# Kernel tuning notes

Hardware: AMD Instinct MI355X
Metric: run time of the kernel (lower is better)

The kernel has to match this reference:

```python
import jax, jax.numpy as jnp
import numpy as np

N_EMBD = 1568  # 2 * 784, hard-coded in the source module
HEAD_SIZE = 128
BATCH = 16384


def setup_inputs() -> dict:
    key = jax.random.key(0)
    kx, kq, kk, kv = jax.random.split(key, 4)
    x = jax.random.normal(kx, (BATCH, N_EMBD), dtype=jnp.float32)
    wq = jax.random.normal(kq, (N_EMBD, HEAD_SIZE), dtype=jnp.float32) * (N_EMBD ** -0.5)
    wk = jax.random.normal(kk, (N_EMBD, HEAD_SIZE), dtype=jnp.float32) * (N_EMBD ** -0.5)
    wv = jax.random.normal(kv, (N_EMBD, HEAD_SIZE), dtype=jnp.float32) * (N_EMBD ** -0.5)
    return {"x": x, "wq": wq, "wk": wk, "wv": wv}


def reference(x, wq, wk, wv):
    # x: [B, N]; projections (bias-free Linear): [B, H]
    B, N = x.shape
    q = x @ wq
    k = x @ wk
    v = x @ wv
    # Outer-product score matrix per batch element: [B, H, H]
    attn = jnp.einsum('bi,bj->bij', q, k) * (N ** -0.5)  # scale uses FEATURE dim N, as in source
    attn = jax.nn.softmax(attn, axis=-1)
    # dropout is identity in eval mode
    out = jnp.einsum('bij,bj->bi', attn, v)  # [B, H]
    return out
```

## Files before the change

kernel.cpp:

```cpp
#include <hip/hip_runtime.h>
#include <stdint.h>

typedef unsigned short u16;
typedef __bf16 bf16x8 __attribute__((ext_vector_type(8)));
typedef float f32x4 __attribute__((ext_vector_type(4)));
typedef float f32x2 __attribute__((ext_vector_type(2)));

#define M_ROWS 16384
#define K_DIM  1568
#define H_DIM  128
#define NQ     384
#define MT     32
#define BK     32
#define NSTEP  49
#define CH_F   384
#define ASTR   392
#define TSTR   40
#define ABUF   (MT * ASTR)
#define PSTR   132
#define KSTRIDE (NQ * BK)
#define SCALE  0.02525381361380526f
#define LOG2E  1.4426950408889634f

__device__ __forceinline__ u16 f32_to_bf16_rne(float f) {
    uint32_t u = __float_as_uint(f);
    uint32_t r = (u + 0x7FFFu + ((u >> 16) & 1u)) >> 16;
    return (u16)r;
}

__device__ __forceinline__ uint32_t cvt_pk(float lo, float hi) {
    uint32_t d;
    asm("v_cvt_pk_bf16_f32 %0, %1, %2" : "=v"(d) : "v"(lo), "v"(hi));
    return d;
}

__device__ __forceinline__ f32x2 pk_mul(f32x2 a, f32x2 b) {
    f32x2 d; asm("v_pk_mul_f32 %0, %1, %2" : "=v"(d) : "v"(a), "v"(b)); return d;
}
__device__ __forceinline__ f32x2 pk_add(f32x2 a, f32x2 b) {
    f32x2 d; asm("v_pk_add_f32 %0, %1, %2" : "=v"(d) : "v"(a), "v"(b)); return d;
}
__device__ __forceinline__ f32x2 pk_fma(f32x2 a, f32x2 b, f32x2 c) {
    f32x2 d; asm("v_pk_fma_f32 %0, %1, %2, %3" : "=v"(d) : "v"(a), "v"(b), "v"(c)); return d;
}

__device__ __forceinline__ void cvt_wr8(u16* dst, f32x4 v) {
    uint2 t; t.x = cvt_pk(v.x, v.y); t.y = cvt_pk(v.z, v.w);
    *(uint2*)dst = t;
}

#define MFMA(a, b, c) __builtin_amdgcn_mfma_f32_16x16x32_bf16(a, b, c, 0, 0, 0)

__global__ __launch_bounds__(256) void wtrans_kernel(
    const float* __restrict__ wq, const float* __restrict__ wk,
    const float* __restrict__ wv, u16* __restrict__ wt2)
{
    __shared__ u16 tile[32][33];
    const float* w = (blockIdx.z == 0) ? wq : (blockIdx.z == 1) ? wk : wv;
    const int k0 = blockIdx.x * 32;
    const int nloc0 = blockIdx.y * 32;
    const int ng0 = blockIdx.z * 128 + nloc0;

    const int tn = threadIdx.x & 31;
    const int tk = threadIdx.x >> 5;
    #pragma unroll
    for (int p = 0; p < 4; p++) {
        int kk = tk + p * 8;
        tile[kk][tn] = f32_to_bf16_rne(w[(size_t)(k0 + kk) * H_DIM + nloc0 + tn]);
    }
    __syncthreads();

    const int klo = threadIdx.x & 31;
    const int tn2 = threadIdx.x >> 5;
    u16* dst = wt2 + (size_t)(k0 >> 5) * KSTRIDE;
    #pragma unroll
    for (int p = 0; p < 4; p++) {
        int nn = tn2 + p * 8;
        dst[(size_t)(ng0 + nn) * 32 + klo] = tile[klo][nn];
    }
}

__global__ __launch_bounds__(512, 4) void fused_kernel(
    const float* __restrict__ x,
    const u16* __restrict__ wt2,
    float* __restrict__ out)
{
    __shared__ char smem[2 * ABUF * 2 + MT * TSTR * 2];
    u16* A0 = (u16*)smem;
    u16* A1 = A0 + ABUF;
    u16* TB = A1 + ABUF;
    float (*Pq)[PSTR] = (float (*)[PSTR])smem;
    float (*Pk)[PSTR] = (float (*)[PSTR])(smem + MT * PSTR * 4);
    float (*Pv)[PSTR] = (float (*)[PSTR])(smem + 2 * MT * PSTR * 4);

    const int tid  = threadIdx.x;
    const int lane = tid & 63;
    const int wave = tid >> 6;
    const int lrow = lane & 15;
    const int quad = lane >> 4;
    const int m0   = blockIdx.x * MT;

    const u16* bp0 = wt2 + (size_t)(wave * 48 +  0 + lrow) * 32 + quad * 8;
    const u16* bp1 = wt2 + (size_t)(wave * 48 + 16 + lrow) * 32 + quad * 8;
    const u16* bp2 = wt2 + (size_t)(wave * 48 + 32 + lrow) * 32 + quad * 8;

    const int srow = tid >> 4;
    const int st16 = tid & 15;
    const float* xrow = x + (size_t)(m0 + srow) * K_DIM;
    u16* wb0 = A0 + srow * ASTR + st16 * 4;
    u16* wb1 = A1 + srow * ASTR + st16 * 4;

    const u16* aA0 = A0 + lrow * ASTR + quad * 8;
    const u16* aA1 = A0 + (16 + lrow) * ASTR + quad * 8;
    const u16* aB0 = A1 + lrow * ASTR + quad * 8;
    const u16* aB1 = A1 + (16 + lrow) * ASTR + quad * 8;

#define NTLD4(off) __builtin_nontemporal_load((const f32x4*)(xrow + (off)))
#define LOADC(S, OFF) do { \
    S##0 = NTLD4((OFF) + st16 * 4 +   0); \
    S##1 = NTLD4((OFF) + st16 * 4 +  64); \
    S##2 = NTLD4((OFF) + st16 * 4 + 128); \
    S##3 = NTLD4((OFF) + st16 * 4 + 192); \
    S##4 = NTLD4((OFF) + st16 * 4 + 256); \
    S##5 = NTLD4((OFF) + st16 * 4 + 320); \
} while (0)
#define WRITEC(WB, S) do { \
    cvt_wr8((WB) +   0, S##0); cvt_wr8((WB) +  64, S##1); \
    cvt_wr8((WB) + 128, S##2); cvt_wr8((WB) + 192, S##3); \
    cvt_wr8((WB) + 256, S##4); cvt_wr8((WB) + 320, S##5); \
} while (0)

    f32x4 acc00 = {}, acc01 = {}, acc02 = {};
    f32x4 acc10 = {}, acc11 = {}, acc12 = {};
    f32x4 s00, s01, s02, s03, s04, s05;
    f32x4 s10, s11, s12, s13, s14, s15;

    LOADC(s0, 0);
    f32x2 tl = __builtin_nontemporal_load((const f32x2*)(xrow + 1536 + st16 * 2));
    LOADC(s1, CH_F);
    WRITEC(wb0, s0);
    *(uint32_t*)(TB + srow * TSTR + st16 * 2) = cvt_pk(tl.x, tl.y);

    bf16x8 Ba0 = *(const bf16x8*)(bp0);
    bf16x8 Ba1 = *(const bf16x8*)(bp1);
    bf16x8 Ba2 = *(const bf16x8*)(bp2);
    bf16x8 Bb0 = *(const bf16x8*)(bp0 + KSTRIDE);
    bf16x8 Bb1 = *(const bf16x8*)(bp1 + KSTRIDE);
    bf16x8 Bb2 = *(const bf16x8*)(bp2 + KSTRIDE);
    __syncthreads();

#define KSTEP(P0, P1, IT, G) do { \
    int gp = (G) + 2; if (gp > NSTEP - 1) gp = NSTEP - 1; \
    const size_t o = (size_t)gp * KSTRIDE; \
    bf16x8 Bc0 = *(const bf16x8*)(bp0 + o); \
    bf16x8 Bc1 = *(const bf16x8*)(bp1 + o); \
    bf16x8 Bc2 = *(const bf16x8*)(bp2 + o); \
    bf16x8 a0 = *(const bf16x8*)((P0) + (IT) * BK); \
    bf16x8 a1 = *(const bf16x8*)((P1) + (IT) * BK); \
    acc00 = MFMA(a0, Ba0, acc00); acc10 = MFMA(a1, Ba0, acc10); \
    acc01 = MFMA(a0, Ba1, acc01); acc11 = MFMA(a1, Ba1, acc11); \
    acc02 = MFMA(a0, Ba2, acc02); acc12 = MFMA(a1, Ba2, acc12); \
    Ba0 = Bb0; Ba1 = Bb1; Ba2 = Bb2; Bb0 = Bc0; Bb1 = Bc1; Bb2 = Bc2; \
} while (0)

    WRITEC(wb1, s1);
    LOADC(s0, 2 * CH_F);
    #pragma unroll
    for (int it = 0; it < 12; ++it) KSTEP(aA0, aA1, it, it);
    __syncthreads();

    WRITEC(wb0, s0);
    LOADC(s1, 3 * CH_F);
    #pragma unroll
    for (int it = 0; it < 12; ++it) KSTEP(aB0, aB1, it, 12 + it);
    __syncthreads();

    WRITEC(wb1, s1);
    #pragma unroll
    for (int it = 0; it < 12; ++it) KSTEP(aA0, aA1, it, 24 + it);
    __syncthreads();

    #pragma unroll
    for (int it = 0; it < 12; ++it) KSTEP(aB0, aB1, it, 36 + it);

    {
        bf16x8 a0 = *(const bf16x8*)(TB + lrow * TSTR + quad * 8);
        bf16x8 a1 = *(const bf16x8*)(TB + (16 + lrow) * TSTR + quad * 8);
        acc00 = MFMA(a0, Ba0, acc00); acc10 = MFMA(a1, Ba0, acc10);
        acc01 = MFMA(a0, Ba1, acc01); acc11 = MFMA(a1, Ba1, acc11);
        acc02 = MFMA(a0, Ba2, acc02); acc12 = MFMA(a1, Ba2, acc12);
    }
    __syncthreads();

#define SCAT(ACC, MTi, NTi) do { \
    const int base = wave * 48 + (NTi) * 16; \
    const int sel  = base >> 7; \
    const int col  = (base & 127) + lrow; \
    const int mrow = (MTi) * 16 + quad * 4; \
    if (sel == 0)      { _Pragma("unroll") for (int rr = 0; rr < 4; rr++) Pq[mrow + rr][col] = ACC[rr] * (SCALE * LOG2E); } \
    else if (sel == 1) { _Pragma("unroll") for (int rr = 0; rr < 4; rr++) Pk[mrow + rr][col] = ACC[rr]; } \
    else               { _Pragma("unroll") for (int rr = 0; rr < 4; rr++) Pv[mrow + rr][col] = ACC[rr]; } \
} while (0)

    SCAT(acc00, 0, 0); SCAT(acc01, 0, 1); SCAT(acc02, 0, 2);
    SCAT(acc10, 1, 0); SCAT(acc11, 1, 1); SCAT(acc12, 1, 2);
    __syncthreads();

    const int r   = tid >> 4;
    const int sub = tid & 15;

    f32x4 qa = *(const f32x4*)&Pq[r][sub * 8];
    f32x4 qb = *(const f32x4*)&Pq[r][sub * 8 + 4];
    f32x2 q01; q01.x = qa.x; q01.y = qa.y;
    f32x2 q23; q23.x = qa.z; q23.y = qa.w;
    f32x2 q45; q45.x = qb.x; q45.y = qb.y;
    f32x2 q67; q67.x = qb.z; q67.y = qb.w;

    f32x2 d01 = {}, d23 = {}, d45 = {}, d67 = {};
    f32x2 n01 = {}, n23 = {}, n45 = {}, n67 = {};

    #pragma unroll 2
    for (int j4 = 0; j4 < 32; ++j4) {
        f32x4 k4 = *(const f32x4*)&Pk[r][j4 * 4];
        f32x4 v4 = *(const f32x4*)&Pv[r][j4 * 4];
        #pragma unroll
        for (int jj = 0; jj < 4; ++jj) {
            float kj = k4[jj];
            float vj = v4[jj];
            f32x2 kk; kk.x = kj; kk.y = kj;
            f32x2 vv; vv.x = vj; vv.y = vj;
            f32x2 sc01 = pk_mul(q01, kk);
            f32x2 sc23 = pk_mul(q23, kk);
            f32x2 sc45 = pk_mul(q45, kk);
            f32x2 sc67 = pk_mul(q67, kk);
            f32x2 e01; e01.x = __builtin_amdgcn_exp2f(sc01.x); e01.y = __builtin_amdgcn_exp2f(sc01.y);
            f32x2 e23; e23.x = __builtin_amdgcn_exp2f(sc23.x); e23.y = __builtin_amdgcn_exp2f(sc23.y);
            f32x2 e45; e45.x = __builtin_amdgcn_exp2f(sc45.x); e45.y = __builtin_amdgcn_exp2f(sc45.y);
            f32x2 e67; e67.x = __builtin_amdgcn_exp2f(sc67.x); e67.y = __builtin_amdgcn_exp2f(sc67.y);
            d01 = pk_add(d01, e01); n01 = pk_fma(e01, vv, n01);
            d23 = pk_add(d23, e23); n23 = pk_fma(e23, vv, n23);
            d45 = pk_add(d45, e45); n45 = pk_fma(e45, vv, n45);
            d67 = pk_add(d67, e67); n67 = pk_fma(e67, vv, n67);
        }
    }

    float* op = out + (size_t)(m0 + r) * H_DIM + sub * 8;
    f32x4 o0, o1;
    o0.x = n01.x / d01.x; o0.y = n01.y / d01.y;
    o0.z = n23.x / d23.x; o0.w = n23.y / d23.y;
    o1.x = n45.x / d45.x; o1.y = n45.y / d45.y;
    o1.z = n67.x / d67.x; o1.w = n67.y / d67.y;
    __builtin_nontemporal_store(o0, (f32x4*)(op));
    __builtin_nontemporal_store(o1, (f32x4*)(op + 4));
}

extern "C" void kernel_launch(void* const* d_in, const int* in_sizes, int n_in,
                              void* d_out, int out_size, void* d_ws, size_t ws_size,
                              hipStream_t stream)
{
    const float* x  = (const float*)d_in[0];
    const float* wq = (const float*)d_in[1];
    const float* wk = (const float*)d_in[2];
    const float* wv = (const float*)d_in[3];
    float* out = (float*)d_out;

    u16* wt2 = (u16*)d_ws;

    wtrans_kernel<<<dim3(K_DIM / 32, H_DIM / 32, 3), 256, 0, stream>>>(wq, wk, wv, wt2);
    fused_kernel<<<M_ROWS / MT, 512, 0, stream>>>(x, wt2, out);
}
```

Before: 204.1 us.

## Double the row tile to 64 and pipeline eight narrower K chunks

Raises the per-block row tile from 32 to 64 so each weight fragment loaded from global memory feeds twice as many MFMAs. This halves weight traffic per row and halves the block count. The K loop is restructured into eight 192-wide chunks with a double-buffered register/LDS pipeline, sized so the staging fits in the reused epilogue buffer. The softmax epilogue now has each thread handle 16 output columns. The cost is more accumulators and registers per thread, occupancy hints lowered from 4 to 2 blocks, and more barriers.

```diff
diff --git a/kernel.cpp b/kernel.cpp
--- a/kernel.cpp
+++ b/kernel.cpp
@@ -10,11 +10,12 @@
 #define K_DIM  1568
 #define H_DIM  128
 #define NQ     384
-#define MT     32
+#define MT     64
 #define BK     32
 #define NSTEP  49
-#define CH_F   384
-#define ASTR   392
+#define NCH    8
+#define CH_F   192
+#define ASTR   200
 #define TSTR   40
 #define ABUF   (MT * ASTR)
 #define PSTR   132
@@ -80,12 +81,12 @@
     }
 }
 
-__global__ __launch_bounds__(512, 4) void fused_kernel(
+__global__ __launch_bounds__(512, 2) void fused_kernel(
     const float* __restrict__ x,
     const u16* __restrict__ wt2,
     float* __restrict__ out)
 {
-    __shared__ char smem[2 * ABUF * 2 + MT * TSTR * 2];
+    __shared__ char smem[3 * MT * PSTR * 4];
     u16* A0 = (u16*)smem;
     u16* A1 = A0 + ABUF;
     u16* TB = A1 + ABUF;
@@ -104,42 +105,46 @@
     const u16* bp1 = wt2 + (size_t)(wave * 48 + 16 + lrow) * 32 + quad * 8;
     const u16* bp2 = wt2 + (size_t)(wave * 48 + 32 + lrow) * 32 + quad * 8;
 
-    const int srow = tid >> 4;
-    const int st16 = tid & 15;
+    const int srow = tid >> 3;
+    const int st8  = tid & 7;
     const float* xrow = x + (size_t)(m0 + srow) * K_DIM;
-    u16* wb0 = A0 + srow * ASTR + st16 * 4;
-    u16* wb1 = A1 + srow * ASTR + st16 * 4;
-
-    const u16* aA0 = A0 + lrow * ASTR + quad * 8;
-    const u16* aA1 = A0 + (16 + lrow) * ASTR + quad * 8;
-    const u16* aB0 = A1 + lrow * ASTR + quad * 8;
-    const u16* aB1 = A1 + (16 + lrow) * ASTR + quad * 8;
+    u16* wbs[2];
+    wbs[0] = A0 + srow * ASTR + st8 * 4;
+    wbs[1] = A1 + srow * ASTR + st8 * 4;
+
+    const u16* aF[2][4];
+    #pragma unroll
+    for (int m = 0; m < 4; m++) {
+        aF[0][m] = A0 + (m * 16 + lrow) * ASTR + quad * 8;
+        aF[1][m] = A1 + (m * 16 + lrow) * ASTR + quad * 8;
+    }
 
 #define NTLD4(off) __builtin_nontemporal_load((const f32x4*)(xrow + (off)))
 #define LOADC(S, OFF) do { \
-    S##0 = NTLD4((OFF) + st16 * 4 +   0); \
-    S##1 = NTLD4((OFF) + st16 * 4 +  64); \
-    S##2 = NTLD4((OFF) + st16 * 4 + 128); \
-    S##3 = NTLD4((OFF) + st16 * 4 + 192); \
-    S##4 = NTLD4((OFF) + st16 * 4 + 256); \
-    S##5 = NTLD4((OFF) + st16 * 4 + 320); \
+    S[0] = NTLD4((OFF) + st8 * 4 +   0); \
+    S[1] = NTLD4((OFF) + st8 * 4 +  32); \
+    S[2] = NTLD4((OFF) + st8 * 4 +  64); \
+    S[3] = NTLD4((OFF) + st8 * 4 +  96); \
+    S[4] = NTLD4((OFF) + st8 * 4 + 128); \
+    S[5] = NTLD4((OFF) + st8 * 4 + 160); \
 } while (0)
 #define WRITEC(WB, S) do { \
-    cvt_wr8((WB) +   0, S##0); cvt_wr8((WB) +  64, S##1); \
-    cvt_wr8((WB) + 128, S##2); cvt_wr8((WB) + 192, S##3); \
-    cvt_wr8((WB) + 256, S##4); cvt_wr8((WB) + 320, S##5); \
+    cvt_wr8((WB) +   0, S[0]); cvt_wr8((WB) +  32, S[1]); \
+    cvt_wr8((WB) +  64, S[2]); cvt_wr8((WB) +  96, S[3]); \
+    cvt_wr8((WB) + 128, S[4]); cvt_wr8((WB) + 160, S[5]); \
 } while (0)
 
     f32x4 acc00 = {}, acc01 = {}, acc02 = {};
     f32x4 acc10 = {}, acc11 = {}, acc12 = {};
-    f32x4 s00, s01, s02, s03, s04, s05;
-    f32x4 s10, s11, s12, s13, s14, s15;
-
-    LOADC(s0, 0);
-    f32x2 tl = __builtin_nontemporal_load((const f32x2*)(xrow + 1536 + st16 * 2));
-    LOADC(s1, CH_F);
-    WRITEC(wb0, s0);
-    *(uint32_t*)(TB + srow * TSTR + st16 * 2) = cvt_pk(tl.x, tl.y);
+    f32x4 acc20 = {}, acc21 = {}, acc22 = {};
+    f32x4 acc30 = {}, acc31 = {}, acc32 = {};
+    f32x4 sreg[2][6];
+
+    LOADC(sreg[0], 0);
+    f32x4 tl = NTLD4(1536 + st8 * 4);
+    LOADC(sreg[1], CH_F);
+    WRITEC(wbs[0], sreg[0]);
+    cvt_wr8(TB + srow * TSTR + st8 * 4, tl);
 
     bf16x8 Ba0 = *(const bf16x8*)(bp0);
     bf16x8 Ba1 = *(const bf16x8*)(bp1);
@@ -149,46 +154,45 @@
     bf16x8 Bb2 = *(const bf16x8*)(bp2 + KSTRIDE);
     __syncthreads();
 
-#define KSTEP(P0, P1, IT, G) do { \
+#define KSTEP(AP, IT, G) do { \
     int gp = (G) + 2; if (gp > NSTEP - 1) gp = NSTEP - 1; \
     const size_t o = (size_t)gp * KSTRIDE; \
     bf16x8 Bc0 = *(const bf16x8*)(bp0 + o); \
     bf16x8 Bc1 = *(const bf16x8*)(bp1 + o); \
     bf16x8 Bc2 = *(const bf16x8*)(bp2 + o); \
-    bf16x8 a0 = *(const bf16x8*)((P0) + (IT) * BK); \
-    bf16x8 a1 = *(const bf16x8*)((P1) + (IT) * BK); \
+    bf16x8 a0 = *(const bf16x8*)((AP)[0] + (IT) * BK); \
+    bf16x8 a1 = *(const bf16x8*)((AP)[1] + (IT) * BK); \
+    bf16x8 a2 = *(const bf16x8*)((AP)[2] + (IT) * BK); \
+    bf16x8 a3 = *(const bf16x8*)((AP)[3] + (IT) * BK); \
     acc00 = MFMA(a0, Ba0, acc00); acc10 = MFMA(a1, Ba0, acc10); \
+    acc20 = MFMA(a2, Ba0, acc20); acc30 = MFMA(a3, Ba0, acc30); \
     acc01 = MFMA(a0, Ba1, acc01); acc11 = MFMA(a1, Ba1, acc11); \
+    acc21 = MFMA(a2, Ba1, acc21); acc31 = MFMA(a3, Ba1, acc31); \
     acc02 = MFMA(a0, Ba2, acc02); acc12 = MFMA(a1, Ba2, acc12); \
+    acc22 = MFMA(a2, Ba2, acc22); acc32 = MFMA(a3, Ba2, acc32); \
     Ba0 = Bb0; Ba1 = Bb1; Ba2 = Bb2; Bb0 = Bc0; Bb1 = Bc1; Bb2 = Bc2; \
 } while (0)
 
-    WRITEC(wb1, s1);
-    LOADC(s0, 2 * CH_F);
-    #pragma unroll
-    for (int it = 0; it < 12; ++it) KSTEP(aA0, aA1, it, it);
-    __syncthreads();
-
-    WRITEC(wb0, s0);
-    LOADC(s1, 3 * CH_F);
-    #pragma unroll
-    for (int it = 0; it < 12; ++it) KSTEP(aB0, aB1, it, 12 + it);
-    __syncthreads();
-
-    WRITEC(wb1, s1);
-    #pragma unroll
-    for (int it = 0; it < 12; ++it) KSTEP(aA0, aA1, it, 24 + it);
-    __syncthreads();
-
-    #pragma unroll
-    for (int it = 0; it < 12; ++it) KSTEP(aB0, aB1, it, 36 + it);
+    #pragma unroll
+    for (int c = 0; c < NCH; ++c) {
+        if (c < NCH - 1) WRITEC(wbs[(c + 1) & 1], sreg[(c + 1) & 1]);
+        if (c < NCH - 2) LOADC(sreg[c & 1], (c + 2) * CH_F);
+        #pragma unroll
+        for (int it = 0; it < 6; ++it) KSTEP(aF[c & 1], it, c * 6 + it);
+        __syncthreads();
+    }
 
     {
-        bf16x8 a0 = *(const bf16x8*)(TB + lrow * TSTR + quad * 8);
-        bf16x8 a1 = *(const bf16x8*)(TB + (16 + lrow) * TSTR + quad * 8);
+        bf16x8 a0 = *(const bf16x8*)(TB + (lrow +  0) * TSTR + quad * 8);
+        bf16x8 a1 = *(const bf16x8*)(TB + (lrow + 16) * TSTR + quad * 8);
+        bf16x8 a2 = *(const bf16x8*)(TB + (lrow + 32) * TSTR + quad * 8);
+        bf16x8 a3 = *(const bf16x8*)(TB + (lrow + 48) * TSTR + quad * 8);
         acc00 = MFMA(a0, Ba0, acc00); acc10 = MFMA(a1, Ba0, acc10);
+        acc20 = MFMA(a2, Ba0, acc20); acc30 = MFMA(a3, Ba0, acc30);
         acc01 = MFMA(a0, Ba1, acc01); acc11 = MFMA(a1, Ba1, acc11);
+        acc21 = MFMA(a2, Ba1, acc21); acc31 = MFMA(a3, Ba1, acc31);
         acc02 = MFMA(a0, Ba2, acc02); acc12 = MFMA(a1, Ba2, acc12);
+        acc22 = MFMA(a2, Ba2, acc22); acc32 = MFMA(a3, Ba2, acc32);
     }
     __syncthreads();
 
@@ -204,20 +208,28 @@
 
     SCAT(acc00, 0, 0); SCAT(acc01, 0, 1); SCAT(acc02, 0, 2);
     SCAT(acc10, 1, 0); SCAT(acc11, 1, 1); SCAT(acc12, 1, 2);
-    __syncthreads();
-
-    const int r   = tid >> 4;
-    const int sub = tid & 15;
-
-    f32x4 qa = *(const f32x4*)&Pq[r][sub * 8];
-    f32x4 qb = *(const f32x4*)&Pq[r][sub * 8 + 4];
-    f32x2 q01; q01.x = qa.x; q01.y = qa.y;
-    f32x2 q23; q23.x = qa.z; q23.y = qa.w;
-    f32x2 q45; q45.x = qb.x; q45.y = qb.y;
-    f32x2 q67; q67.x = qb.z; q67.y = qb.w;
-
-    f32x2 d01 = {}, d23 = {}, d45 = {}, d67 = {};
-    f32x2 n01 = {}, n23 = {}, n45 = {}, n67 = {};
+    SCAT(acc20, 2, 0); SCAT(acc21, 2, 1); SCAT(acc22, 2, 2);
+    SCAT(acc30, 3, 0); SCAT(acc31, 3, 1); SCAT(acc32, 3, 2);
+    __syncthreads();
+
+    const int r   = tid >> 3;
+    const int sub = tid & 7;
+
+    f32x4 qa = *(const f32x4*)&Pq[r][sub * 16 +  0];
+    f32x4 qb = *(const f32x4*)&Pq[r][sub * 16 +  4];
+    f32x4 qc = *(const f32x4*)&Pq[r][sub * 16 +  8];
+    f32x4 qd = *(const f32x4*)&Pq[r][sub * 16 + 12];
+    f32x2 qp0; qp0.x = qa.x; qp0.y = qa.y;
+    f32x2 qp1; qp1.x = qa.z; qp1.y = qa.w;
+    f32x2 qp2; qp2.x = qb.x; qp2.y = qb.y;
+    f32x2 qp3; qp3.x = qb.z; qp3.y = qb.w;
+    f32x2 qp4; qp4.x = qc.x; qp4.y = qc.y;
+    f32x2 qp5; qp5.x = qc.z; qp5.y = qc.w;
+    f32x2 qp6; qp6.x = qd.x; qp6.y = qd.y;
+    f32x2 qp7; qp7.x = qd.z; qp7.y = qd.w;
+
+    f32x2 d0 = {}, d1 = {}, d2 = {}, d3 = {}, d4 = {}, d5 = {}, d6 = {}, d7 = {};
+    f32x2 n0 = {}, n1 = {}, n2 = {}, n3 = {}, n4 = {}, n5 = {}, n6 = {}, n7 = {};
 
     #pragma unroll 2
     for (int j4 = 0; j4 < 32; ++j4) {
@@ -229,29 +241,43 @@
             float vj = v4[jj];
             f32x2 kk; kk.x = kj; kk.y = kj;
             f32x2 vv; vv.x = vj; vv.y = vj;
-            f32x2 sc01 = pk_mul(q01, kk);
-            f32x2 sc23 = pk_mul(q23, kk);
-            f32x2 sc45 = pk_mul(q45, kk);
-            f32x2 sc67 = pk_mul(q67, kk);
-            f32x2 e01; e01.x = __builtin_amdgcn_exp2f(sc01.x); e01.y = __builtin_amdgcn_exp2f(sc01.y);
-            f32x2 e23; e23.x = __builtin_amdgcn_exp2f(sc23.x); e23.y = __builtin_amdgcn_exp2f(sc23.y);
-            f32x2 e45; e45.x = __builtin_amdgcn_exp2f(sc45.x); e45.y = __builtin_amdgcn_exp2f(sc45.y);
-            f32x2 e67; e67.x = __builtin_amdgcn_exp2f(sc67.x); e67.y = __builtin_amdgcn_exp2f(sc67.y);
-            d01 = pk_add(d01, e01); n01 = pk_fma(e01, vv, n01);
-            d23 = pk_add(d23, e23); n23 = pk_fma(e23, vv, n23);
-            d45 = pk_add(d45, e45); n45 = pk_fma(e45, vv, n45);
-            d67 = pk_add(d67, e67); n67 = pk_fma(e67, vv, n67);
+            f32x2 s0 = pk_mul(qp0, kk);
+            f32x2 s1 = pk_mul(qp1, kk);
+            f32x2 s2 = pk_mul(qp2, kk);
+            f32x2 s3 = pk_mul(qp3, kk);
+            f32x2 s4 = pk_mul(qp4, kk);
+            f32x2 s5 = pk_mul(qp5, kk);
+            f32x2 s6 = pk_mul(qp6, kk);
+            f32x2 s7 = pk_mul(qp7, kk);
+            f32x2 e0; e0.x = __builtin_amdgcn_exp2f(s0.x); e0.y = __builtin_amdgcn_exp2f(s0.y);
+            f32x2 e1; e1.x = __builtin_amdgcn_exp2f(s1.x); e1.y = __builtin_amdgcn_exp2f(s1.y);
+            f32x2 e2; e2.x = __builtin_amdgcn_exp2f(s2.x); e2.y = __builtin_amdgcn_exp2f(s2.y);
+            f32x2 e3; e3.x = __builtin_amdgcn_exp2f(s3.x); e3.y = __builtin_amdgcn_exp2f(s3.y);
+            f32x2 e4; e4.x = __builtin_amdgcn_exp2f(s4.x); e4.y = __builtin_amdgcn_exp2f(s4.y);
+            f32x2 e5; e5.x = __builtin_amdgcn_exp2f(s5.x); e5.y = __builtin_amdgcn_exp2f(s5.y);
+            f32x2 e6; e6.x = __builtin_amdgcn_exp2f(s6.x); e6.y = __builtin_amdgcn_exp2f(s6.y);
+            f32x2 e7; e7.x = __builtin_amdgcn_exp2f(s7.x); e7.y = __builtin_amdgcn_exp2f(s7.y);
+            d0 = pk_add(d0, e0); n0 = pk_fma(e0, vv, n0);
+            d1 = pk_add(d1, e1); n1 = pk_fma(e1, vv, n1);
+            d2 = pk_add(d2, e2); n2 = pk_fma(e2, vv, n2);
+            d3 = pk_add(d3, e3); n3 = pk_fma(e3, vv, n3);
+            d4 = pk_add(d4, e4); n4 = pk_fma(e4, vv, n4);
+            d5 = pk_add(d5, e5); n5 = pk_fma(e5, vv, n5);
+            d6 = pk_add(d6, e6); n6 = pk_fma(e6, vv, n6);
+            d7 = pk_add(d7, e7); n7 = pk_fma(e7, vv, n7);
         }
     }
 
-    float* op = out + (size_t)(m0 + r) * H_DIM + sub * 8;
-    f32x4 o0, o1;
-    o0.x = n01.x / d01.x; o0.y = n01.y / d01.y;
-    o0.z = n23.x / d23.x; o0.w = n23.y / d23.y;
-    o1.x = n45.x / d45.x; o1.y = n45.y / d45.y;
-    o1.z = n67.x / d67.x; o1.w = n67.y / d67.y;
-    __builtin_nontemporal_store(o0, (f32x4*)(op));
-    __builtin_nontemporal_store(o1, (f32x4*)(op + 4));
+    float* op = out + (size_t)(m0 + r) * H_DIM + sub * 16;
+    f32x4 o0, o1, o2, o3;
+    o0.x = n0.x / d0.x; o0.y = n0.y / d0.y; o0.z = n1.x / d1.x; o0.w = n1.y / d1.y;
+    o1.x = n2.x / d2.x; o1.y = n2.y / d2.y; o1.z = n3.x / d3.x; o1.w = n3.y / d3.y;
+    o2.x = n4.x / d4.x; o2.y = n4.y / d4.y; o2.z = n5.x / d5.x; o2.w = n5.y / d5.y;
+    o3.x = n6.x / d6.x; o3.y = n6.y / d6.y; o3.z = n7.x / d7.x; o3.w = n7.y / d7.y;
+    __builtin_nontemporal_store(o0, (f32x4*)(op +  0));
+    __builtin_nontemporal_store(o1, (f32x4*)(op +  4));
+    __builtin_nontemporal_store(o2, (f32x4*)(op +  8));
+    __builtin_nontemporal_store(o3, (f32x4*)(op + 12));
 }
 
 extern "C" void kernel_launch(void* const* d_in, const int* in_sizes, int n_in,
```

Result: faster. 195.9 us (-4.1%).
